# Optimization experiments

Hardware: AMD Instinct MI355X
Metric: run time of the kernel (lower is better)

The kernel has to match this reference:

```python
import jax, jax.numpy as jnp
import numpy as np

FEAT_DIM = 2048
NUM_CLASSES = 1000
BATCH = 8192
REACH_SCALE = 10.0
COS_SCALE = 16.0


def setup_inputs() -> dict:
    key = jax.random.key(0)
    ks = jax.random.split(key, 7)
    x = jax.random.normal(ks[0], (BATCH, FEAT_DIM), dtype=jnp.float32)
    centroids = jax.random.normal(ks[1], (NUM_CLASSES, FEAT_DIM), dtype=jnp.float32)
    # nn.Linear-style params (W: [out, in], b: [out]), small init scale
    s_h = 1.0 / np.sqrt(FEAT_DIM)
    W_hall = jax.random.uniform(ks[2], (NUM_CLASSES, FEAT_DIM), jnp.float32, -s_h, s_h)
    b_hall = jax.random.uniform(ks[3], (NUM_CLASSES,), jnp.float32, -s_h, s_h)
    W_sel = jax.random.uniform(ks[4], (FEAT_DIM, FEAT_DIM), jnp.float32, -s_h, s_h)
    b_sel = jax.random.uniform(ks[5], (FEAT_DIM,), jnp.float32, -s_h, s_h)
    # CosNorm_Classifier weight: [num_classes, feat_dim]
    W_cos = jax.random.uniform(ks[6], (NUM_CLASSES, FEAT_DIM), jnp.float32, -s_h, s_h)
    return {"x": x, "centroids": centroids, "W_hall": W_hall, "b_hall": b_hall,
            "W_sel": W_sel, "b_sel": b_sel, "W_cos": W_cos}


def reference(x, centroids, W_hall, b_hall, W_sel, b_sel, W_cos):
    # --- min Euclidean distance to centroids via the matmul identity ---
    x_sq = jnp.sum(x * x, axis=1, keepdims=True)               # [B, 1]
    c_sq = jnp.sum(centroids * centroids, axis=1)[None, :]     # [1, C]
    d2 = x_sq + c_sq - 2.0 * (x @ centroids.T)                 # [B, C]
    min_dist = jnp.sqrt(jnp.maximum(jnp.min(d2, axis=1), 0.0)) # [B]
    reachability = (REACH_SCALE / min_dist)[:, None]           # [B, 1] (broadcasts over feat)

    # --- hallucinated memory attention over class centroids ---
    values_memory = jax.nn.softmax(x @ W_hall.T + b_hall, axis=1)  # [B, C]
    memory_feature = values_memory @ centroids                     # [B, D]

    # --- gated fusion ---
    concept_selector = jnp.tanh(x @ W_sel.T + b_sel)               # [B, D]
    infused_feature = concept_selector * memory_feature            # [B, D]
    fused = reachability * (x + infused_feature)                   # [B, D]

    # --- CosNorm classifier: scale * (|x|/(1+|x|)) * (x/|x|) @ (W/|W|)^T ---
    norm_x = jnp.linalg.norm(fused, axis=1, keepdims=True)         # [B, 1]
    ex = (norm_x / (1.0 + norm_x)) * (fused / norm_x)              # [B, D]
    ew = W_cos / jnp.linalg.norm(W_cos, axis=1, keepdims=True)     # [C, D]
    logits = COS_SCALE * (ex @ ew.T)                               # [B, C]

    direct_feature = x
    return logits, direct_feature, infused_feature
```

## Files before the change

kernel.cpp:

```cpp
#include <hip/hip_runtime.h>
#include <hip/hip_bf16.h>

typedef __bf16 bf16x8 __attribute__((ext_vector_type(8)));
typedef float  f32x4  __attribute__((ext_vector_type(4)));
typedef unsigned short u16;

__device__ __forceinline__ u16 f2bf(float f) {
    __hip_bfloat16 h = __float2bfloat16(f);
    return __builtin_bit_cast(unsigned short, h);
}

template <int MODE>
__device__ __forceinline__ float blockReduce(float v, float* sbuf) {
    #pragma unroll
    for (int off = 32; off > 0; off >>= 1) {
        float o = __shfl_down(v, off, 64);
        v = (MODE == 0) ? v + o : (MODE == 1) ? fmaxf(v, o) : fminf(v, o);
    }
    int lane = threadIdx.x & 63, w = threadIdx.x >> 6;
    __syncthreads();
    if (lane == 0) sbuf[w] = v;
    __syncthreads();
    float r = sbuf[0];
    #pragma unroll
    for (int i = 1; i < 4; ++i) {
        float o = sbuf[i];
        r = (MODE == 0) ? r + o : (MODE == 1) ? fmaxf(r, o) : fminf(r, o);
    }
    return r;
}

__global__ void convert_rowsq(const float* __restrict__ src, u16* __restrict__ dst,
                              float* __restrict__ rowsq, int validRows) {
    __shared__ float sbuf[4];
    int r = blockIdx.x, t = threadIdx.x;
    size_t base = (size_t)r * 2048 + t * 8;
    float ss = 0.f;
    ushort4 u0 = {0,0,0,0}, u1 = {0,0,0,0};
    if (r < validRows) {
        float4 a0 = *(const float4*)(src + base);
        float4 a1 = *(const float4*)(src + base + 4);
        ss = a0.x*a0.x + a0.y*a0.y + a0.z*a0.z + a0.w*a0.w
           + a1.x*a1.x + a1.y*a1.y + a1.z*a1.z + a1.w*a1.w;
        u0.x = f2bf(a0.x); u0.y = f2bf(a0.y); u0.z = f2bf(a0.z); u0.w = f2bf(a0.w);
        u1.x = f2bf(a1.x); u1.y = f2bf(a1.y); u1.z = f2bf(a1.z); u1.w = f2bf(a1.w);
    }
    *(ushort4*)(dst + base)     = u0;
    *(ushort4*)(dst + base + 4) = u1;
    if (rowsq != nullptr) {
        ss = blockReduce<0>(ss, sbuf);
        if (t == 0) rowsq[r] = ss;
    }
}

__global__ void norm_rows(const float* __restrict__ src, u16* __restrict__ dst, int validRows) {
    __shared__ float sbuf[4];
    int r = blockIdx.x, t = threadIdx.x;
    size_t base = (size_t)r * 2048 + t * 8;
    ushort4 u0 = {0,0,0,0}, u1 = {0,0,0,0};
    if (r < validRows) {
        float4 a0 = *(const float4*)(src + base);
        float4 a1 = *(const float4*)(src + base + 4);
        float ss = a0.x*a0.x + a0.y*a0.y + a0.z*a0.z + a0.w*a0.w
                 + a1.x*a1.x + a1.y*a1.y + a1.z*a1.z + a1.w*a1.w;
        ss = blockReduce<0>(ss, sbuf);
        float sc = 1.f / sqrtf(ss);
        u0.x = f2bf(a0.x*sc); u0.y = f2bf(a0.y*sc); u0.z = f2bf(a0.z*sc); u0.w = f2bf(a0.w*sc);
        u1.x = f2bf(a1.x*sc); u1.y = f2bf(a1.y*sc); u1.z = f2bf(a1.z*sc); u1.w = f2bf(a1.w*sc);
    }
    *(ushort4*)(dst + base)     = u0;
    *(ushort4*)(dst + base + 4) = u1;
}

__global__ void transpose_to_bf16(const float* __restrict__ src, u16* __restrict__ dst, int validRows) {
    __shared__ u16 tile[32][33];
    int d0 = blockIdx.x * 32;
    int c0 = blockIdx.y * 32;
    int tx = threadIdx.x, ty = threadIdx.y;
    #pragma unroll
    for (int k = 0; k < 4; ++k) {
        int c = c0 + ty + k * 8;
        float v = (c < validRows) ? src[(size_t)c * 2048 + d0 + tx] : 0.f;
        tile[ty + k * 8][tx] = f2bf(v);
    }
    __syncthreads();
    #pragma unroll
    for (int k = 0; k < 4; ++k) {
        int d = d0 + ty + k * 8;
        dst[(size_t)d * 1024 + c0 + tx] = tile[tx][ty + k * 8];
    }
}

template <int EPI>
__global__ __launch_bounds__(256, 2)
void gemm_bt(const u16* __restrict__ A, const u16* __restrict__ Bt, float* __restrict__ C,
             int K, int ldc, int nValid,
             const float* __restrict__ bias, const float* __restrict__ aux) {
    __shared__ u16 As[128 * 64];
    __shared__ u16 Bs[128 * 64];
    const int tid  = threadIdx.x;
    const int lane = tid & 63;
    const int w    = tid >> 6;
    const int wr   = w >> 1, wc = w & 1;
    const int quad = lane >> 4, r16 = lane & 15;
    const int sw   = r16 & 7;
    const int lr   = lane >> 3;
    const int lc   = lane & 7;
    const int lk   = (lc ^ lr) * 8;
    const size_t rowBase = (size_t)blockIdx.y * 128;
    const size_t colBase = (size_t)blockIdx.x * 128;

    f32x4 acc[4][4] = {};

    for (int kt = 0; kt < K; kt += 64) {
        #pragma unroll
        for (int i = 0; i < 4; ++i) {
            int ci = w * 4 + i;
            const u16* ga = A  + (rowBase + ci * 8 + lr) * (size_t)K + kt + lk;
            const u16* gb = Bt + (colBase + ci * 8 + lr) * (size_t)K + kt + lk;
            __builtin_amdgcn_global_load_lds(
                (const __attribute__((address_space(1))) void*)ga,
                (__attribute__((address_space(3))) void*)(As + ci * 512), 16, 0, 0);
            __builtin_amdgcn_global_load_lds(
                (const __attribute__((address_space(1))) void*)gb,
                (__attribute__((address_space(3))) void*)(Bs + ci * 512), 16, 0, 0);
        }
        __syncthreads();
        #pragma unroll
        for (int kk2 = 0; kk2 < 2; ++kk2) {
            const int off = (((kk2 << 2) | quad) ^ sw) * 8;
            bf16x8 a[4], b[4];
            #pragma unroll
            for (int i = 0; i < 4; ++i)
                a[i] = *(const bf16x8*)(As + (wr * 64 + i * 16 + r16) * 64 + off);
            #pragma unroll
            for (int j = 0; j < 4; ++j)
                b[j] = *(const bf16x8*)(Bs + (wc * 64 + j * 16 + r16) * 64 + off);
            #pragma unroll
            for (int i = 0; i < 4; ++i)
                #pragma unroll
                for (int j = 0; j < 4; ++j)
                    acc[i][j] = __builtin_amdgcn_mfma_f32_16x16x32_bf16(a[i], b[j], acc[i][j], 0, 0, 0);
        }
        __syncthreads();
    }

    #pragma unroll
    for (int i = 0; i < 4; ++i) {
        #pragma unroll
        for (int j = 0; j < 4; ++j) {
            #pragma unroll
            for (int v = 0; v < 4; ++v) {
                size_t grow = rowBase + wr * 64 + i * 16 + quad * 4 + v;
                size_t gcol = colBase + wc * 64 + j * 16 + r16;
                float val = acc[i][j][v];
                if (EPI == 0) {
                    C[grow * (size_t)ldc + gcol] = val;
                } else if (EPI == 2) {
                    float t = tanhf(val + bias[gcol]);
                    C[grow * (size_t)ldc + gcol] = t * aux[grow * (size_t)ldc + gcol];
                } else if (EPI == 3) {
                    if ((int)gcol < nValid) C[grow * (size_t)ldc + gcol] = 16.0f * val;
                }
            }
        }
    }
}

__global__ void min_reach(const float* __restrict__ S, const float* __restrict__ xsq,
                          const float* __restrict__ csq, float* __restrict__ reach) {
    __shared__ float sbuf[4];
    int r = blockIdx.x, t = threadIdx.x;
    float m = 1e30f;
    for (int c = t; c < 1000; c += 256)
        m = fminf(m, csq[c] - 2.f * S[(size_t)r * 2048 + c]);
    m = blockReduce<2>(m, sbuf);
    if (t == 0) {
        float d2 = xsq[r] + m;
        reach[r] = 10.f / sqrtf(fmaxf(d2, 0.f));
    }
}

__global__ void softmax_vm(const float* __restrict__ S, const float* __restrict__ bh,
                           u16* __restrict__ Vm) {
    __shared__ float sbuf[4];
    int r = blockIdx.x, t = threadIdx.x;
    float l[4];
    float m = -1e30f;
    #pragma unroll
    for (int i = 0; i < 4; ++i) {
        int c = t + i * 256;
        l[i] = (c < 1000) ? (S[(size_t)r * 2048 + 1024 + c] + bh[c]) : -1e30f;
        m = fmaxf(m, l[i]);
    }
    m = blockReduce<1>(m, sbuf);
    float s = 0.f;
    #pragma unroll
    for (int i = 0; i < 4; ++i) {
        int c = t + i * 256;
        l[i] = (c < 1000) ? expf(l[i] - m) : 0.f;
        s += l[i];
    }
    s = blockReduce<0>(s, sbuf);
    float inv = 1.f / s;
    #pragma unroll
    for (int i = 0; i < 4; ++i) {
        int c = t + i * 256;
        Vm[(size_t)r * 1024 + c] = f2bf(l[i] * inv);
    }
}

__global__ void fuse_ex(const float* __restrict__ x, const float* __restrict__ inf,
                        const float* __restrict__ reach, u16* __restrict__ exh) {
    __shared__ float sbuf[4];
    int r = blockIdx.x, t = threadIdx.x;
    size_t base = (size_t)r * 2048 + t * 8;
    float4 a0 = *(const float4*)(x + base),   a1 = *(const float4*)(x + base + 4);
    float4 b0 = *(const float4*)(inf + base), b1 = *(const float4*)(inf + base + 4);
    float rr = reach[r];
    float f[8];
    f[0] = rr * (a0.x + b0.x); f[1] = rr * (a0.y + b0.y);
    f[2] = rr * (a0.z + b0.z); f[3] = rr * (a0.w + b0.w);
    f[4] = rr * (a1.x + b1.x); f[5] = rr * (a1.y + b1.y);
    f[6] = rr * (a1.z + b1.z); f[7] = rr * (a1.w + b1.w);
    float ss = 0.f;
    #pragma unroll
    for (int i = 0; i < 8; ++i) ss += f[i] * f[i];
    ss = blockReduce<0>(ss, sbuf);
    float sc = 1.f / (1.f + sqrtf(ss));
    ushort4 u0, u1;
    u0.x = f2bf(f[0]*sc); u0.y = f2bf(f[1]*sc); u0.z = f2bf(f[2]*sc); u0.w = f2bf(f[3]*sc);
    u1.x = f2bf(f[4]*sc); u1.y = f2bf(f[5]*sc); u1.z = f2bf(f[6]*sc); u1.w = f2bf(f[7]*sc);
    *(ushort4*)(exh + base)     = u0;
    *(ushort4*)(exh + base + 4) = u1;
}

extern "C" void kernel_launch(void* const* d_in, const int* in_sizes, int n_in,
                              void* d_out, int out_size, void* d_ws, size_t ws_size,
                              hipStream_t stream) {
    const float* x      = (const float*)d_in[0];
    const float* cent   = (const float*)d_in[1];
    const float* W_hall = (const float*)d_in[2];
    const float* b_hall = (const float*)d_in[3];
    const float* W_sel  = (const float*)d_in[4];
    const float* b_sel  = (const float*)d_in[5];
    const float* W_cos  = (const float*)d_in[6];

    float* out_logits = (float*)d_out;
    float* out_x      = out_logits + (size_t)8192 * 1000;
    float* out_inf    = out_x      + (size_t)8192 * 2048;

    char* ws = (char*)d_ws;
    u16*   xh      = (u16*)  (ws);
    u16*   cent_bt = (u16*)  (ws + 33554432);
    u16*   whall   = (u16*)  (ws + 37748736);
    u16*   wsel    = (u16*)  (ws + 41943040);
    u16*   ew      = (u16*)  (ws + 50331648);
    u16*   centT   = (u16*)  (ws + 54525952);
    float* S       = (float*)(ws + 58720256);
    u16*   Vm      = (u16*)  (ws + 125829120);
    float* xsq     = (float*)(ws + 142606336);
    float* csq     = (float*)(ws + 142639104);
    float* reach   = (float*)(ws + 142643200);
    float* memf    = S;
    u16*   exh     = xh;

    (void)in_sizes; (void)n_in; (void)out_size; (void)ws_size;

    hipMemcpyAsync(out_x, x, (size_t)8192 * 2048 * 4, hipMemcpyDeviceToDevice, stream);

    convert_rowsq<<<8192, 256, 0, stream>>>(x, xh, xsq, 8192);
    convert_rowsq<<<1024, 256, 0, stream>>>(cent, cent_bt, csq, 1000);
    convert_rowsq<<<1024, 256, 0, stream>>>(W_hall, whall, nullptr, 1000);
    convert_rowsq<<<2048, 256, 0, stream>>>(W_sel, wsel, nullptr, 2048);
    norm_rows<<<1024, 256, 0, stream>>>(W_cos, ew, 1000);
    transpose_to_bf16<<<dim3(64, 32), dim3(32, 8), 0, stream>>>(cent, centT, 1000);

    gemm_bt<0><<<dim3(16, 64), 256, 0, stream>>>(xh, cent_bt, S, 2048, 2048, 0, nullptr, nullptr);
    min_reach<<<8192, 256, 0, stream>>>(S, xsq, csq, reach);
    softmax_vm<<<8192, 256, 0, stream>>>(S, b_hall, Vm);

    gemm_bt<0><<<dim3(16, 64), 256, 0, stream>>>(Vm, centT, memf, 1024, 2048, 0, nullptr, nullptr);

    gemm_bt<2><<<dim3(16, 64), 256, 0, stream>>>(xh, wsel, out_inf, 2048, 2048, 0, b_sel, memf);

    fuse_ex<<<8192, 256, 0, stream>>>(x, out_inf, reach, exh);

    gemm_bt<3><<<dim3(8, 64), 256, 0, stream>>>(exh, ew, out_logits, 2048, 1000, 1000, nullptr, nullptr);
}
```

Before: 566.6 us.

## Fuse x copy, min/softmax, and fused-feature production into GEMM epilogues

The passthrough copy of x now happens inside the bf16 conversion kernel, and the min-distance and softmax kernels are merged into one. The W_sel GEMM epilogue now also writes the reach-scaled fused feature in bf16. A small row-norm kernel computes a per-row cosine scale that the final GEMM applies in its epilogue, replacing the fp32 re-read in fuse_ex. This removes several full passes over 8192x2048 fp32 data, at the cost of computing the norm from bf16-rounded x and fused values, which slightly changes precision.

```diff
diff --git a/kernel.cpp b/kernel.cpp
--- a/kernel.cpp
+++ b/kernel.cpp
@@ -8,6 +8,9 @@
 __device__ __forceinline__ u16 f2bf(float f) {
     __hip_bfloat16 h = __float2bfloat16(f);
     return __builtin_bit_cast(unsigned short, h);
+}
+__device__ __forceinline__ float bf2f(u16 u) {
+    return __bfloat162float(__builtin_bit_cast(__hip_bfloat16, u));
 }
 
 template <int MODE>
@@ -31,15 +34,17 @@
 }
 
 __global__ void convert_rowsq(const float* __restrict__ src, u16* __restrict__ dst,
-                              float* __restrict__ rowsq, int validRows) {
+                              float* __restrict__ rowsq, float* __restrict__ copyOut,
+                              int validRows) {
     __shared__ float sbuf[4];
     int r = blockIdx.x, t = threadIdx.x;
     size_t base = (size_t)r * 2048 + t * 8;
     float ss = 0.f;
     ushort4 u0 = {0,0,0,0}, u1 = {0,0,0,0};
+    float4 a0 = {0,0,0,0}, a1 = {0,0,0,0};
     if (r < validRows) {
-        float4 a0 = *(const float4*)(src + base);
-        float4 a1 = *(const float4*)(src + base + 4);
+        a0 = *(const float4*)(src + base);
+        a1 = *(const float4*)(src + base + 4);
         ss = a0.x*a0.x + a0.y*a0.y + a0.z*a0.z + a0.w*a0.w
            + a1.x*a1.x + a1.y*a1.y + a1.z*a1.z + a1.w*a1.w;
         u0.x = f2bf(a0.x); u0.y = f2bf(a0.y); u0.z = f2bf(a0.z); u0.w = f2bf(a0.w);
@@ -47,6 +52,10 @@
     }
     *(ushort4*)(dst + base)     = u0;
     *(ushort4*)(dst + base + 4) = u1;
+    if (copyOut != nullptr) {
+        *(float4*)(copyOut + base)     = a0;
+        *(float4*)(copyOut + base + 4) = a1;
+    }
     if (rowsq != nullptr) {
         ss = blockReduce<0>(ss, sbuf);
         if (t == 0) rowsq[r] = ss;
@@ -95,7 +104,9 @@
 __global__ __launch_bounds__(256, 2)
 void gemm_bt(const u16* __restrict__ A, const u16* __restrict__ Bt, float* __restrict__ C,
              int K, int ldc, int nValid,
-             const float* __restrict__ bias, const float* __restrict__ aux) {
+             const float* __restrict__ bias, const float* __restrict__ aux,
+             const float* __restrict__ reach, const u16* __restrict__ xh2,
+             u16* __restrict__ fusedh) {
     __shared__ u16 As[128 * 64];
     __shared__ u16 Bs[128 * 64];
     const int tid  = threadIdx.x;
@@ -157,18 +168,23 @@
                 if (EPI == 0) {
                     C[grow * (size_t)ldc + gcol] = val;
                 } else if (EPI == 2) {
-                    float t = tanhf(val + bias[gcol]);
-                    C[grow * (size_t)ldc + gcol] = t * aux[grow * (size_t)ldc + gcol];
+                    float t   = tanhf(val + bias[gcol]);
+                    float inf = t * aux[grow * (size_t)ldc + gcol];
+                    C[grow * (size_t)ldc + gcol] = inf;
+                    float xv = bf2f(xh2[grow * (size_t)ldc + gcol]);
+                    float fu = reach[grow] * (xv + inf);
+                    fusedh[grow * (size_t)ldc + gcol] = f2bf(fu);
                 } else if (EPI == 3) {
-                    if ((int)gcol < nValid) C[grow * (size_t)ldc + gcol] = 16.0f * val;
+                    if ((int)gcol < nValid) C[grow * (size_t)ldc + gcol] = bias[grow] * val;
                 }
             }
         }
     }
 }
 
-__global__ void min_reach(const float* __restrict__ S, const float* __restrict__ xsq,
-                          const float* __restrict__ csq, float* __restrict__ reach) {
+__global__ void min_softmax(const float* __restrict__ S, const float* __restrict__ xsq,
+                            const float* __restrict__ csq, const float* __restrict__ bh,
+                            float* __restrict__ reach, u16* __restrict__ Vm) {
     __shared__ float sbuf[4];
     int r = blockIdx.x, t = threadIdx.x;
     float m = 1e30f;
@@ -179,26 +195,20 @@
         float d2 = xsq[r] + m;
         reach[r] = 10.f / sqrtf(fmaxf(d2, 0.f));
     }
-}
-
-__global__ void softmax_vm(const float* __restrict__ S, const float* __restrict__ bh,
-                           u16* __restrict__ Vm) {
-    __shared__ float sbuf[4];
-    int r = blockIdx.x, t = threadIdx.x;
     float l[4];
-    float m = -1e30f;
+    float mx = -1e30f;
     #pragma unroll
     for (int i = 0; i < 4; ++i) {
         int c = t + i * 256;
         l[i] = (c < 1000) ? (S[(size_t)r * 2048 + 1024 + c] + bh[c]) : -1e30f;
-        m = fmaxf(m, l[i]);
-    }
-    m = blockReduce<1>(m, sbuf);
+        mx = fmaxf(mx, l[i]);
+    }
+    mx = blockReduce<1>(mx, sbuf);
     float s = 0.f;
     #pragma unroll
     for (int i = 0; i < 4; ++i) {
         int c = t + i * 256;
-        l[i] = (c < 1000) ? expf(l[i] - m) : 0.f;
+        l[i] = (c < 1000) ? expf(l[i] - mx) : 0.f;
         s += l[i];
     }
     s = blockReduce<0>(s, sbuf);
@@ -210,29 +220,17 @@
     }
 }
 
-__global__ void fuse_ex(const float* __restrict__ x, const float* __restrict__ inf,
-                        const float* __restrict__ reach, u16* __restrict__ exh) {
+__global__ void rowsq_scale(const u16* __restrict__ fusedh, float* __restrict__ scale) {
     __shared__ float sbuf[4];
     int r = blockIdx.x, t = threadIdx.x;
     size_t base = (size_t)r * 2048 + t * 8;
-    float4 a0 = *(const float4*)(x + base),   a1 = *(const float4*)(x + base + 4);
-    float4 b0 = *(const float4*)(inf + base), b1 = *(const float4*)(inf + base + 4);
-    float rr = reach[r];
-    float f[8];
-    f[0] = rr * (a0.x + b0.x); f[1] = rr * (a0.y + b0.y);
-    f[2] = rr * (a0.z + b0.z); f[3] = rr * (a0.w + b0.w);
-    f[4] = rr * (a1.x + b1.x); f[5] = rr * (a1.y + b1.y);
-    f[6] = rr * (a1.z + b1.z); f[7] = rr * (a1.w + b1.w);
-    float ss = 0.f;
-    #pragma unroll
-    for (int i = 0; i < 8; ++i) ss += f[i] * f[i];
+    ushort4 u0 = *(const ushort4*)(fusedh + base);
+    ushort4 u1 = *(const ushort4*)(fusedh + base + 4);
+    float f0 = bf2f(u0.x), f1 = bf2f(u0.y), f2 = bf2f(u0.z), f3 = bf2f(u0.w);
+    float f4 = bf2f(u1.x), f5 = bf2f(u1.y), f6 = bf2f(u1.z), f7 = bf2f(u1.w);
+    float ss = f0*f0 + f1*f1 + f2*f2 + f3*f3 + f4*f4 + f5*f5 + f6*f6 + f7*f7;
     ss = blockReduce<0>(ss, sbuf);
-    float sc = 1.f / (1.f + sqrtf(ss));
-    ushort4 u0, u1;
-    u0.x = f2bf(f[0]*sc); u0.y = f2bf(f[1]*sc); u0.z = f2bf(f[2]*sc); u0.w = f2bf(f[3]*sc);
-    u1.x = f2bf(f[4]*sc); u1.y = f2bf(f[5]*sc); u1.z = f2bf(f[6]*sc); u1.w = f2bf(f[7]*sc);
-    *(ushort4*)(exh + base)     = u0;
-    *(ushort4*)(exh + base + 4) = u1;
+    if (t == 0) scale[r] = 16.f / (1.f + sqrtf(ss));
 }
 
 extern "C" void kernel_launch(void* const* d_in, const int* in_sizes, int n_in,
@@ -262,29 +260,31 @@
     float* xsq     = (float*)(ws + 142606336);
     float* csq     = (float*)(ws + 142639104);
     float* reach   = (float*)(ws + 142643200);
+    float* scale   = (float*)(ws + 142675968);
+    u16*   fusedh  = (u16*)  (ws + 142708736);
     float* memf    = S;
-    u16*   exh     = xh;
 
     (void)in_sizes; (void)n_in; (void)out_size; (void)ws_size;
 
-    hipMemcpyAsync(out_x, x, (size_t)8192 * 2048 * 4, hipMemcpyDeviceToDevice, stream);
-
-    convert_rowsq<<<8192, 256, 0, stream>>>(x, xh, xsq, 8192);
-    convert_rowsq<<<1024, 256, 0, stream>>>(cent, cent_bt, csq, 1000);
-    convert_rowsq<<<1024, 256, 0, stream>>>(W_hall, whall, nullptr, 1000);
-    convert_rowsq<<<2048, 256, 0, stream>>>(W_sel, wsel, nullptr, 2048);
+    convert_rowsq<<<8192, 256, 0, stream>>>(x, xh, xsq, out_x, 8192);
+    convert_rowsq<<<1024, 256, 0, stream>>>(cent, cent_bt, csq, nullptr, 1000);
+    convert_rowsq<<<1024, 256, 0, stream>>>(W_hall, whall, nullptr, nullptr, 1000);
+    convert_rowsq<<<2048, 256, 0, stream>>>(W_sel, wsel, nullptr, nullptr, 2048);
     norm_rows<<<1024, 256, 0, stream>>>(W_cos, ew, 1000);
     transpose_to_bf16<<<dim3(64, 32), dim3(32, 8), 0, stream>>>(cent, centT, 1000);
 
-    gemm_bt<0><<<dim3(16, 64), 256, 0, stream>>>(xh, cent_bt, S, 2048, 2048, 0, nullptr, nullptr);
-    min_reach<<<8192, 256, 0, stream>>>(S, xsq, csq, reach);
-    softmax_vm<<<8192, 256, 0, stream>>>(S, b_hall, Vm);
-
-    gemm_bt<0><<<dim3(16, 64), 256, 0, stream>>>(Vm, centT, memf, 1024, 2048, 0, nullptr, nullptr);
-
-    gemm_bt<2><<<dim3(16, 64), 256, 0, stream>>>(xh, wsel, out_inf, 2048, 2048, 0, b_sel, memf);
-
-    fuse_ex<<<8192, 256, 0, stream>>>(x, out_inf, reach, exh);
-
-    gemm_bt<3><<<dim3(8, 64), 256, 0, stream>>>(exh, ew, out_logits, 2048, 1000, 1000, nullptr, nullptr);
-}
+    gemm_bt<0><<<dim3(16, 64), 256, 0, stream>>>(xh, cent_bt, S, 2048, 2048, 0,
+                                                 nullptr, nullptr, nullptr, nullptr, nullptr);
+    min_softmax<<<8192, 256, 0, stream>>>(S, xsq, csq, b_hall, reach, Vm);
+
+    gemm_bt<0><<<dim3(16, 64), 256, 0, stream>>>(Vm, centT, memf, 1024, 2048, 0,
+                                                 nullptr, nullptr, nullptr, nullptr, nullptr);
+
+    gemm_bt<2><<<dim3(16, 64), 256, 0, stream>>>(xh, wsel, out_inf, 2048, 2048, 0,
+                                                 b_sel, memf, reach, xh, fusedh);
+
+    rowsq_scale<<<8192, 256, 0, stream>>>(fusedh, scale);
+
+    gemm_bt<3><<<dim3(8, 64), 256, 0, stream>>>(fusedh, ew, out_logits, 2048, 1000, 1000,
+                                                scale, nullptr, nullptr, nullptr, nullptr);
+}
```

After: 553.0 us. -2.4%, faster.
